# Kernel optimization log

Hardware: AMD Instinct MI355X
Metric: run time of the kernel (lower is better)

## Reference

```python
import jax, jax.numpy as jnp
import numpy as np

B, T, V, E, H, LAT, L = 2048, 120, 64, 128, 512, 256, 2


def setup_inputs() -> dict:
    key = jax.random.key(0)
    ks = jax.random.split(key, 16)
    s = 0.05  # weight init scale
    z = jax.random.normal(ks[0], (B, LAT), jnp.float32)
    target = jax.random.randint(ks[1], (B, T), 0, V)
    embed = (jax.random.normal(ks[2], (V, E), jnp.float32) * s).at[0].set(0.0)  # padding_idx=0
    fc_hidden_w = jax.random.normal(ks[3], (H * L, LAT), jnp.float32) * s
    fc_hidden_b = jax.random.normal(ks[4], (H * L,), jnp.float32) * s
    W_ih0 = jax.random.normal(ks[5], (3 * H, E + LAT), jnp.float32) * s
    W_hh0 = jax.random.normal(ks[6], (3 * H, H), jnp.float32) * s
    b_ih0 = jax.random.normal(ks[7], (3 * H,), jnp.float32) * s
    b_hh0 = jax.random.normal(ks[8], (3 * H,), jnp.float32) * s
    W_ih1 = jax.random.normal(ks[9], (3 * H, H), jnp.float32) * s
    W_hh1 = jax.random.normal(ks[10], (3 * H, H), jnp.float32) * s
    b_ih1 = jax.random.normal(ks[11], (3 * H,), jnp.float32) * s
    b_hh1 = jax.random.normal(ks[12], (3 * H,), jnp.float32) * s
    fc_out_w = jax.random.normal(ks[13], (V, H), jnp.float32) * s
    fc_out_b = jax.random.normal(ks[14], (V,), jnp.float32) * s
    return dict(z=z, target=target, embed=embed, fc_hidden_w=fc_hidden_w,
                fc_hidden_b=fc_hidden_b, W_ih0=W_ih0, W_hh0=W_hh0, b_ih0=b_ih0,
                b_hh0=b_hh0, W_ih1=W_ih1, W_hh1=W_hh1, b_ih1=b_ih1, b_hh1=b_hh1,
                fc_out_w=fc_out_w, fc_out_b=fc_out_b)


def _gru_cell(x, h, W_ih, W_hh, b_ih, b_hh):
    # torch GRU cell: r,z,n gate ordering
    gx = x @ W_ih.T + b_ih          # [B, 3H]
    gh = h @ W_hh.T + b_hh          # [B, 3H]
    xr, xz, xn = jnp.split(gx, 3, axis=-1)
    hr, hz, hn = jnp.split(gh, 3, axis=-1)
    r = jax.nn.sigmoid(xr + hr)
    u = jax.nn.sigmoid(xz + hz)
    n = jnp.tanh(xn + r * hn)
    return (1.0 - u) * n + u * h


def reference(z, target, embed, fc_hidden_w, fc_hidden_b, W_ih0, W_hh0, b_ih0,
              b_hh0, W_ih1, W_hh1, b_ih1, b_hh1, fc_out_w, fc_out_b):
    b, lat = z.shape
    t = target.shape[1]
    hd = W_hh0.shape[1]
    # initial hidden: fc_hidden(z).view(B, L, H) -> per-layer states
    hid = (z @ fc_hidden_w.T + fc_hidden_b).reshape(b, L, hd)
    h0, h1 = hid[:, 0, :], hid[:, 1, :]
    # teacher forcing with ratio 1.0: input_0 = token 1, input_t = target[:, t-1]
    tok = jnp.concatenate([jnp.ones((b, 1), target.dtype), target[:, :-1]], axis=1)
    # precompute per-step GRU inputs: [T, B, E+LAT]
    xs = jnp.concatenate(
        [embed[tok], jnp.broadcast_to(z[:, None, :], (b, t, lat))], axis=-1)
    xs = jnp.swapaxes(xs, 0, 1)

    def step(carry, x):
        h0, h1 = carry
        h0n = _gru_cell(x, h0, W_ih0, W_hh0, b_ih0, b_hh0)
        h1n = _gru_cell(h0n, h1, W_ih1, W_hh1, b_ih1, b_hh1)
        logits = h1n @ fc_out_w.T + fc_out_b
        return (h0n, h1n), logits

    _, out = jax.lax.scan(step, (h0, h1), xs)   # [T, B, V]
    return jnp.swapaxes(out, 0, 1)              # [B, T, V]
```

## Files before the change

kernel.cpp:

```cpp
#include <hip/hip_runtime.h>
#include <hip/hip_bf16.h>

#define DI __device__ __forceinline__

typedef short bf16x8 __attribute__((ext_vector_type(8)));
typedef float f32x4 __attribute__((ext_vector_type(4)));

constexpr int B_ = 2048, T_ = 120, V_ = 64, E_ = 128, H_ = 512, LAT_ = 256;
constexpr int H3 = 1536;

DI short f2b(float f) {
  union { __hip_bfloat16 h; short s; } u;
  u.h = __float2bfloat16(f);
  return u.s;
}
DI float b2f(short s) {
  union { unsigned u; float f; } x;
  x.u = (unsigned)(unsigned short)s << 16;
  return x.f;
}
DI float sigm(float x) { return 1.f / (1.f + __expf(-x)); }
DI float tanh_f(float x) {
  x = fminf(15.f, fmaxf(-15.f, x));
  float e = __expf(2.f * x);
  return (e - 1.f) / (e + 1.f);
}
DI float gru_one(float xr, float xz, float xn, float hr, float hz, float hn, float hp) {
  float r = sigm(xr + hr);
  float u = sigm(xz + hz);
  float nn = tanh_f(xn + r * hn);
  return (1.f - u) * nn + u * hp;
}
DI float gru_pre(float sr, float sz, float xn, float hn, float hp) {
  float r = sigm(sr);
  float u = sigm(sz);
  float nn = tanh_f(xn + r * hn);
  return (1.f - u) * nn + u * hp;
}

template <int ROWS, int BK, int NV>
DI void rs_load(const short* __restrict__ G, int row0, int K, int kk, bf16x8 (&v)[NV]) {
  constexpr int SLOTS = BK / 8;
  constexpr int RPP = 2048 / BK;
  static_assert(NV == ROWS / RPP, "NV mismatch");
  const int tid = threadIdx.x;
  const int rl = tid / SLOTS, sl = tid % SLOTS;
#pragma unroll
  for (int p = 0; p < NV; ++p)
    v[p] = *(const bf16x8*)(G + (size_t)(row0 + p * RPP + rl) * K + kk + sl * 8);
}
template <int ROWS, int BK, int NV>
DI void rs_write(char* __restrict__ lds, bf16x8 (&v)[NV]) {
  constexpr int SLOTS = BK / 8;
  constexpr int RPP = 2048 / BK;
  const int tid = threadIdx.x;
  const int rl = tid / SLOTS, sl = tid % SLOTS;
#pragma unroll
  for (int p = 0; p < NV; ++p) {
    int row = p * RPP + rl;
    *(bf16x8*)(lds + row * (SLOTS * 16) + ((sl ^ (row & (SLOTS - 1))) * 16)) = v[p];
  }
}
template <int BK>
DI bf16x8 fragL(const char* __restrict__ lds, int row, int kk) {
  return *(const bf16x8*)(lds + row * (BK * 2) + ((kk << 1) ^ ((row & (BK / 8 - 1)) << 4)));
}

DI void gemm_core(const short* __restrict__ A, const short* __restrict__ Bw,
                  int arow, int bcol, char* lds, f32x4 (&acc)[2][4]) {
  char* As[2] = {lds, lds + 8192};
  char* Bs[2] = {lds + 16384, lds + 32768};
  const int tid = threadIdx.x, lane = tid & 63, wid = tid >> 6;
  const int wm = wid >> 1, wn = wid & 1;
  const int r = lane & 15, ko = (lane >> 4) * 8;
  bf16x8 va[2], vb[4];
  rs_load<64, 64, 2>(A, arow, H_, 0, va);
  rs_load<128, 64, 4>(Bw, bcol, H_, 0, vb);
  rs_write<64, 64, 2>(As[0], va);
  rs_write<128, 64, 4>(Bs[0], vb);
  __syncthreads();
  int cur = 0;
  for (int c = 0; c < 8; ++c) {
    if (c < 7) {
      rs_load<64, 64, 2>(A, arow, H_, (c + 1) * 64, va);
      rs_load<128, 64, 4>(Bw, bcol, H_, (c + 1) * 64, vb);
    }
#pragma unroll
    for (int kh = 0; kh < 2; ++kh) {
      const int kkk = kh * 32 + ko;
      bf16x8 a[2], b[4];
#pragma unroll
      for (int i = 0; i < 2; ++i) a[i] = fragL<64>(As[cur], wm * 32 + i * 16 + r, kkk);
#pragma unroll
      for (int j = 0; j < 4; ++j) b[j] = fragL<64>(Bs[cur], wn * 64 + j * 16 + r, kkk);
#pragma unroll
      for (int i = 0; i < 2; ++i)
#pragma unroll
        for (int j = 0; j < 4; ++j)
          acc[i][j] = __builtin_amdgcn_mfma_f32_16x16x32_bf16(a[i], b[j], acc[i][j], 0, 0, 0);
    }
    if (c < 7) {
      rs_write<64, 64, 2>(As[cur ^ 1], va);
      rs_write<128, 64, 4>(Bs[cur ^ 1], vb);
    }
    __syncthreads();
    cur ^= 1;
  }
}

struct GArgs {
  const short* zgx; const short* egx; const int* target;
  float* h0f; float* h1f; short* h0b; short* h1b;
  short* p0;
  short* gx1a; short* gx1b;
  short* gh1;
  const short* Wb_hh0; const float* b_hh0;
  const short* Wb_ih1; const float* b_ih1;
  const short* Wb_hh1; const float* b_hh1;
  const short* Wb_out; const float* fc_out_b;
  float* out;
};

__global__ __launch_bounds__(256) void k_A(GArgs a, int t) {
  extern __shared__ char smem[];
  const int u = blockIdx.x;
  const int tid = threadIdx.x, lane = tid & 63, wid = tid >> 6;
  if (u < 384) {
    if (t >= T_) return;
    const int mt = u / 12, nt = u % 12;
    const int arow = mt * 64, bcol = nt * 128;
    f32x4 acc[2][4] = {};
    gemm_core(a.h0b, a.Wb_hh0, arow, bcol, smem, acc);
    const int wm = wid >> 1, wn = wid & 1;
    const int r0 = (lane >> 4) * 4, c0 = lane & 15;
    const int g = nt >> 2;
#pragma unroll
    for (int i = 0; i < 2; ++i)
#pragma unroll
      for (int j = 0; j < 4; ++j) {
        const int col = bcol + wn * 64 + j * 16 + c0;
        const int jj = col & 511;
        const float bv = a.b_hh0[col];
#pragma unroll
        for (int rr = 0; rr < 4; ++rr) {
          const int row = arow + wm * 32 + i * 16 + r0 + rr;
          const float val = acc[i][j][rr] + bv;
          const int tok = (t == 0) ? 1 : a.target[(size_t)row * T_ + (t - 1)];
          const float xv = b2f(a.zgx[(size_t)row * H3 + g * 512 + jj]) +
                           b2f(a.egx[(size_t)tok * H3 + g * 512 + jj]);
          short* pr = a.p0 + ((size_t)row * 4) * 512 + jj;
          if (g < 2) {
            pr[g * 512] = f2b(val + xv);
          } else {
            pr[2 * 512] = f2b(xv);
            pr[3 * 512] = f2b(val);
          }
        }
      }
    return;
  }
  if (u < 768) {
    if (t < 1 || t > T_) return;
    short* gxw = ((t - 1) & 1) ? a.gx1b : a.gx1a;
    const int uu = u - 384;
    const int mt = uu / 12, nt = uu % 12;
    const int arow = mt * 64, bcol = nt * 128;
    f32x4 acc[2][4] = {};
    gemm_core(a.h0b, a.Wb_ih1, arow, bcol, smem, acc);
    const int wm = wid >> 1, wn = wid & 1;
    const int r0 = (lane >> 4) * 4, c0 = lane & 15;
#pragma unroll
    for (int i = 0; i < 2; ++i)
#pragma unroll
      for (int j = 0; j < 4; ++j) {
        const int col = bcol + wn * 64 + j * 16 + c0;
        const float bv = a.b_ih1[col];
#pragma unroll
        for (int rr = 0; rr < 4; ++rr)
          gxw[(size_t)(arow + wm * 32 + i * 16 + r0 + rr) * H3 + col] = f2b(acc[i][j][rr] + bv);
      }
    return;
  }
  if (t < 2) return;
  const short* gxr = (t & 1) ? a.gx1b : a.gx1a;
  short* sh = (short*)smem;
  const int row0 = (u - 768) * 16;
  const int tlog = t - 2;
#pragma unroll 1
  for (int c = 0; c < 4; ++c) {
    int f = c * 2048 + tid * 8;
    int rl = f >> 9, j = f & 511;
    int row = row0 + rl;
    const short* gx = gxr + (size_t)row * H3 + j;
    const short* gh = a.gh1 + (size_t)row * H3 + j;
    float* hf = a.h1f + (size_t)row * H_ + j;
    bf16x8 xr = *(const bf16x8*)(gx);
    bf16x8 xz = *(const bf16x8*)(gx + H_);
    bf16x8 xn = *(const bf16x8*)(gx + 2 * H_);
    bf16x8 hr = *(const bf16x8*)(gh);
    bf16x8 hz = *(const bf16x8*)(gh + H_);
    bf16x8 hn = *(const bf16x8*)(gh + 2 * H_);
    float4 hp0 = *(const float4*)(hf);
    float4 hp1 = *(const float4*)(hf + 4);
    float hp[8] = {hp0.x, hp0.y, hp0.z, hp0.w, hp1.x, hp1.y, hp1.z, hp1.w};
    float hv[8];
    bf16x8 ov;
#pragma unroll
    for (int e = 0; e < 8; ++e) {
      hv[e] = gru_one(b2f(xr[e]), b2f(xz[e]), b2f(xn[e]),
                      b2f(hr[e]), b2f(hz[e]), b2f(hn[e]), hp[e]);
      ov[e] = f2b(hv[e]);
    }
    *(float4*)(hf) = make_float4(hv[0], hv[1], hv[2], hv[3]);
    *(float4*)(hf + 4) = make_float4(hv[4], hv[5], hv[6], hv[7]);
    *(bf16x8*)(a.h1b + (size_t)row * H_ + j) = ov;
    *(bf16x8*)(&sh[rl * 520 + j]) = ov;
  }
  __syncthreads();
  const int w = tid >> 6;
  const int c0 = lane & 15, ko = (lane >> 4) * 8;
  f32x4 acc = {};
  const short* wb = a.Wb_out + (size_t)(w * 16 + c0) * H_ + ko;
  const short* ap = &sh[c0 * 520 + ko];
#pragma unroll
  for (int m = 0; m < 16; ++m) {
    bf16x8 av = *(const bf16x8*)(ap + m * 32);
    bf16x8 bw = *(const bf16x8*)(wb + m * 32);
    acc = __builtin_amdgcn_mfma_f32_16x16x32_bf16(av, bw, acc, 0, 0, 0);
  }
  const int r0 = (lane >> 4) * 4;
  const int col = w * 16 + c0;
  const float bv = a.fc_out_b[col];
#pragma unroll
  for (int rr = 0; rr < 4; ++rr) {
    int brow = row0 + r0 + rr;
    a.out[((size_t)brow * T_ + tlog) * V_ + col] = acc[rr] + bv;
  }
}

__global__ __launch_bounds__(256) void k_C(GArgs a, int t) {
  extern __shared__ char smem[];
  const int u = blockIdx.x;
  const int tid = threadIdx.x;
  if (u < 128) {
    if (t >= T_) return;
    const int row0 = u * 16;
#pragma unroll 1
    for (int it = 0; it < 4; ++it) {
      int v = it * 256 + tid;
      int rl = v >> 6, jb = v & 63;
      int row = row0 + rl, j = jb * 8;
      const short* pr = a.p0 + ((size_t)row * 4) * 512 + j;
      bf16x8 sr = *(const bf16x8*)(pr);
      bf16x8 sz = *(const bf16x8*)(pr + 512);
      bf16x8 xn = *(const bf16x8*)(pr + 1024);
      bf16x8 hn = *(const bf16x8*)(pr + 1536);
      float* hf = a.h0f + (size_t)row * H_ + j;
      float4 hp0 = *(const float4*)(hf);
      float4 hp1 = *(const float4*)(hf + 4);
      float hp[8] = {hp0.x, hp0.y, hp0.z, hp0.w, hp1.x, hp1.y, hp1.z, hp1.w};
      float hv[8];
      bf16x8 ov;
#pragma unroll
      for (int e = 0; e < 8; ++e) {
        hv[e] = gru_pre(b2f(sr[e]), b2f(sz[e]), b2f(xn[e]), b2f(hn[e]), hp[e]);
        ov[e] = f2b(hv[e]);
      }
      *(float4*)(hf) = make_float4(hv[0], hv[1], hv[2], hv[3]);
      *(float4*)(hf + 4) = make_float4(hv[4], hv[5], hv[6], hv[7]);
      *(bf16x8*)(a.h0b + (size_t)row * H_ + j) = ov;
    }
    return;
  }
  if (t < 1 || t > T_) return;
  const int uu = u - 128;
  const int mt = uu / 12, nt = uu % 12;
  const int arow = mt * 64, bcol = nt * 128;
  f32x4 acc[2][4] = {};
  gemm_core(a.h1b, a.Wb_hh1, arow, bcol, smem, acc);
  const int lane = tid & 63, wid = tid >> 6;
  const int wm = wid >> 1, wn = wid & 1;
  const int r0 = (lane >> 4) * 4, c0 = lane & 15;
#pragma unroll
  for (int i = 0; i < 2; ++i)
#pragma unroll
    for (int j = 0; j < 4; ++j) {
      const int col = bcol + wn * 64 + j * 16 + c0;
      const float bv = a.b_hh1[col];
#pragma unroll
      for (int rr = 0; rr < 4; ++rr)
        a.gh1[(size_t)(arow + wm * 32 + i * 16 + r0 + rr) * H3 + col] = f2b(acc[i][j][rr] + bv);
    }
}

template <int MI, int NJ>
DI void gemm_wave_global(const short* __restrict__ A, const short* __restrict__ B,
                         const int K, const int arow, const int bcol,
                         f32x4 (&acc)[MI][NJ]) {
  const int lane = threadIdx.x & 63;
  const int r = lane & 15, ko = (lane >> 4) * 8;
  const short* Ap = A + (size_t)(arow + r) * K + ko;
  const short* Bp = B + (size_t)(bcol + r) * K + ko;
  for (int kk = 0; kk < K; kk += 32) {
    bf16x8 a[MI], b[NJ];
#pragma unroll
    for (int i = 0; i < MI; ++i) a[i] = *(const bf16x8*)(Ap + (size_t)i * 16 * K + kk);
#pragma unroll
    for (int j = 0; j < NJ; ++j) b[j] = *(const bf16x8*)(Bp + (size_t)j * 16 * K + kk);
#pragma unroll
    for (int i = 0; i < MI; ++i)
#pragma unroll
      for (int j = 0; j < NJ; ++j)
        acc[i][j] = __builtin_amdgcn_mfma_f32_16x16x32_bf16(a[i], b[j], acc[i][j], 0, 0, 0);
  }
}
template <int MI, int NJ>
DI void epi_store_bf16(short* __restrict__ C, const float* __restrict__ bias,
                       const int N, const int arow, const int bcol, f32x4 (&acc)[MI][NJ]) {
  const int lane = threadIdx.x & 63;
  const int r0 = (lane >> 4) * 4, c0 = lane & 15;
#pragma unroll
  for (int i = 0; i < MI; ++i)
#pragma unroll
    for (int j = 0; j < NJ; ++j) {
      int col = bcol + j * 16 + c0;
      float bv = bias[col];
#pragma unroll
      for (int rr = 0; rr < 4; ++rr)
        C[(size_t)(arow + i * 16 + r0 + rr) * N + col] = f2b(acc[i][j][rr] + bv);
    }
}

__global__ __launch_bounds__(256) void k_prep0(
    const float* __restrict__ W_hh0, const float* __restrict__ W_ih1,
    const float* __restrict__ W_hh1, const float* __restrict__ fc_out_w,
    const float* __restrict__ W_ih0, const float* __restrict__ fc_hidden_w,
    const float* __restrict__ z,
    short* Wb_hh0, short* Wb_ih1, short* Wb_hh1, short* Wb_out,
    short* Wb_ih0z, short* Wb_fch, short* z_b) {
  const int n1 = H3 * H_;
  const int n2 = V_ * H_;
  const int n3 = H3 * LAT_;
  const int n4 = (2 * H_) * LAT_;
  const int n5 = B_ * LAT_;
  const int total = n1 * 3 + n2 + n3 + n4 + n5;
  for (int i = blockIdx.x * blockDim.x + threadIdx.x; i < total;
       i += gridDim.x * blockDim.x) {
    int idx = i;
    if (idx < n1) { Wb_hh0[idx] = f2b(W_hh0[idx]); continue; }
    idx -= n1;
    if (idx < n1) { Wb_ih1[idx] = f2b(W_ih1[idx]); continue; }
    idx -= n1;
    if (idx < n1) { Wb_hh1[idx] = f2b(W_hh1[idx]); continue; }
    idx -= n1;
    if (idx < n2) { Wb_out[idx] = f2b(fc_out_w[idx]); continue; }
    idx -= n2;
    if (idx < n3) {
      int n = idx >> 8, k = idx & 255;
      Wb_ih0z[idx] = f2b(W_ih0[(size_t)n * (E_ + LAT_) + E_ + k]);
      continue;
    }
    idx -= n3;
    if (idx < n4) { Wb_fch[idx] = f2b(fc_hidden_w[idx]); continue; }
    idx -= n4;
    z_b[idx] = f2b(z[idx]);
  }
}

__global__ __launch_bounds__(256) void k_prep_emb(const float* __restrict__ embed,
                                                  const float* __restrict__ W_ih0,
                                                  short* __restrict__ egx) {
  __shared__ float er[E_];
  int v = blockIdx.x;
  for (int e = threadIdx.x; e < E_; e += blockDim.x) er[e] = embed[(size_t)v * E_ + e];
  __syncthreads();
  for (int n = threadIdx.x; n < H3; n += blockDim.x) {
    const float* w = W_ih0 + (size_t)n * (E_ + LAT_);
    float acc = 0.f;
#pragma unroll 8
    for (int e = 0; e < E_; ++e) acc += er[e] * w[e];
    egx[(size_t)v * H3 + n] = f2b(acc);
  }
}

__global__ __launch_bounds__(256) void k_prep1(
    const short* __restrict__ z_b, const short* __restrict__ Wb_ih0z,
    const short* __restrict__ Wb_fch, const float* __restrict__ b_ih0,
    const float* __restrict__ fc_hidden_b,
    short* zgx, float* h0f, float* h1f, short* h0b, short* h1b) {
  const int bid = blockIdx.x;
  const int mtile = bid / 20, ntile = bid % 20;
  const int tid = threadIdx.x, lane = tid & 63, wid = tid >> 6;
  const int wm = wid >> 1, wn = wid & 1;
  const int arow = mtile * 128 + wm * 64;
  f32x4 acc[4][4] = {};
  if (ntile < 12) {
    int bcol = ntile * 128 + wn * 64;
    gemm_wave_global<4, 4>(z_b, Wb_ih0z, LAT_, arow, bcol, acc);
    epi_store_bf16<4, 4>(zgx, b_ih0, H3, arow, bcol, acc);
  } else {
    int bcol = (ntile - 12) * 128 + wn * 64;
    gemm_wave_global<4, 4>(z_b, Wb_fch, LAT_, arow, bcol, acc);
    const int r0 = (lane >> 4) * 4, c0 = lane & 15;
#pragma unroll
    for (int i = 0; i < 4; ++i)
#pragma unroll
      for (int j = 0; j < 4; ++j) {
        int col = bcol + j * 16 + c0;
        float bv = fc_hidden_b[col];
#pragma unroll
        for (int rr = 0; rr < 4; ++rr) {
          int row = arow + i * 16 + r0 + rr;
          float v = acc[i][j][rr] + bv;
          if (col < H_) {
            h0f[(size_t)row * H_ + col] = v;
            h0b[(size_t)row * H_ + col] = f2b(v);
          } else {
            h1f[(size_t)row * H_ + (col - H_)] = v;
            h1b[(size_t)row * H_ + (col - H_)] = f2b(v);
          }
        }
      }
  }
}

extern "C" void kernel_launch(void* const* d_in, const int* in_sizes, int n_in,
                              void* d_out, int out_size, void* d_ws, size_t ws_size,
                              hipStream_t stream) {
  const float* z           = (const float*)d_in[0];
  const int*   target      = (const int*)d_in[1];
  const float* embed       = (const float*)d_in[2];
  const float* fc_hidden_w = (const float*)d_in[3];
  const float* fc_hidden_b = (const float*)d_in[4];
  const float* W_ih0       = (const float*)d_in[5];
  const float* W_hh0       = (const float*)d_in[6];
  const float* b_ih0       = (const float*)d_in[7];
  const float* b_hh0       = (const float*)d_in[8];
  const float* W_ih1       = (const float*)d_in[9];
  const float* W_hh1       = (const float*)d_in[10];
  const float* b_ih1       = (const float*)d_in[11];
  const float* b_hh1       = (const float*)d_in[12];
  const float* fc_out_w    = (const float*)d_in[13];
  const float* fc_out_b    = (const float*)d_in[14];
  float* out = (float*)d_out;

  char* ws = (char*)d_ws;
  size_t off = 0;
  auto alloc = [&](size_t bytes) -> void* {
    off = (off + 255) & ~(size_t)255;
    void* p = ws + off;
    off += bytes;
    return p;
  };
  float* h0f    = (float*)alloc((size_t)B_ * H_ * 4);
  float* h1f    = (float*)alloc((size_t)B_ * H_ * 4);
  short* h0b    = (short*)alloc((size_t)B_ * H_ * 2);
  short* h1b    = (short*)alloc((size_t)B_ * H_ * 2);
  short* p0     = (short*)alloc((size_t)B_ * 4 * H_ * 2);
  short* gx1a   = (short*)alloc((size_t)B_ * H3 * 2);
  short* gx1b   = (short*)alloc((size_t)B_ * H3 * 2);
  short* gh1    = (short*)alloc((size_t)B_ * H3 * 2);
  short* zgx    = (short*)alloc((size_t)B_ * H3 * 2);
  short* egx    = (short*)alloc((size_t)V_ * H3 * 2);
  short* Wb_hh0 = (short*)alloc((size_t)H3 * H_ * 2);
  short* Wb_ih1 = (short*)alloc((size_t)H3 * H_ * 2);
  short* Wb_hh1 = (short*)alloc((size_t)H3 * H_ * 2);
  short* Wb_out = (short*)alloc((size_t)V_ * H_ * 2);
  short* Wb_ih0z= (short*)alloc((size_t)H3 * LAT_ * 2);
  short* Wb_fch = (short*)alloc((size_t)2 * H_ * LAT_ * 2);
  short* z_b    = (short*)alloc((size_t)B_ * LAT_ * 2);
  if (off > ws_size) return;

  k_prep0<<<2048, 256, 0, stream>>>(W_hh0, W_ih1, W_hh1, fc_out_w, W_ih0, fc_hidden_w,
                                    z, Wb_hh0, Wb_ih1, Wb_hh1, Wb_out, Wb_ih0z, Wb_fch, z_b);
  k_prep_emb<<<64, 256, 0, stream>>>(embed, W_ih0, egx);
  k_prep1<<<320, 256, 0, stream>>>(z_b, Wb_ih0z, Wb_fch, b_ih0, fc_hidden_b,
                                   zgx, h0f, h1f, h0b, h1b);

  GArgs a;
  a.zgx = zgx; a.egx = egx; a.target = target;
  a.h0f = h0f; a.h1f = h1f; a.h0b = h0b; a.h1b = h1b;
  a.p0 = p0; a.gx1a = gx1a; a.gx1b = gx1b; a.gh1 = gh1;
  a.Wb_hh0 = Wb_hh0; a.b_hh0 = b_hh0;
  a.Wb_ih1 = Wb_ih1; a.b_ih1 = b_ih1;
  a.Wb_hh1 = Wb_hh1; a.b_hh1 = b_hh1;
  a.Wb_out = Wb_out; a.fc_out_b = fc_out_b;
  a.out = out;

  for (int t = 0; t <= T_ + 1; ++t) {
    k_A<<<896, 256, 49152, stream>>>(a, t);
    if (t <= T_) k_C<<<512, 256, 49152, stream>>>(a, t);
  }
}
```

Measured before the change: 4.389 ms.

## Restructure recurrent schedule into two per-step kernels, dropping gx1 double buffer

The per-timestep work is regrouped so one kernel runs all three GEMMs (hh0, ih1, hh1), with the layer-0 GEMM pairs interleaved per row group. The second kernel does the layer-0 and layer-1 pointwise GRU updates plus the output projection. The pipeline lag shrinks from two steps to one, so the loop runs one fewer iteration and the double-buffered gx1 becomes a single buffer. The second kernel uses only 256 blocks and a smaller shared allocation. Merging the three GEMMs into a 1152-block launch raises per-launch parallelism, at the cost of a different dependency staging between layers.

```diff
diff --git a/kernel.cpp b/kernel.cpp
--- a/kernel.cpp
+++ b/kernel.cpp
@@ -112,8 +112,7 @@
   const short* zgx; const short* egx; const int* target;
   float* h0f; float* h1f; short* h0b; short* h1b;
   short* p0;
-  short* gx1a; short* gx1b;
-  short* gh1;
+  short* gx1; short* gh1;
   const short* Wb_hh0; const float* b_hh0;
   const short* Wb_ih1; const float* b_ih1;
   const short* Wb_hh1; const float* b_hh1;
@@ -121,124 +120,83 @@
   float* out;
 };
 
-__global__ __launch_bounds__(256) void k_A(GArgs a, int t) {
+__global__ __launch_bounds__(256) void k_L1(GArgs a, int t) {
   extern __shared__ char smem[];
   const int u = blockIdx.x;
   const int tid = threadIdx.x, lane = tid & 63, wid = tid >> 6;
-  if (u < 384) {
-    if (t >= T_) return;
-    const int mt = u / 12, nt = u % 12;
-    const int arow = mt * 64, bcol = nt * 128;
-    f32x4 acc[2][4] = {};
-    gemm_core(a.h0b, a.Wb_hh0, arow, bcol, smem, acc);
-    const int wm = wid >> 1, wn = wid & 1;
-    const int r0 = (lane >> 4) * 4, c0 = lane & 15;
-    const int g = nt >> 2;
-#pragma unroll
-    for (int i = 0; i < 2; ++i)
-#pragma unroll
-      for (int j = 0; j < 4; ++j) {
-        const int col = bcol + wn * 64 + j * 16 + c0;
-        const int jj = col & 511;
-        const float bv = a.b_hh0[col];
-#pragma unroll
-        for (int rr = 0; rr < 4; ++rr) {
-          const int row = arow + wm * 32 + i * 16 + r0 + rr;
-          const float val = acc[i][j][rr] + bv;
-          const int tok = (t == 0) ? 1 : a.target[(size_t)row * T_ + (t - 1)];
-          const float xv = b2f(a.zgx[(size_t)row * H3 + g * 512 + jj]) +
-                           b2f(a.egx[(size_t)tok * H3 + g * 512 + jj]);
-          short* pr = a.p0 + ((size_t)row * 4) * 512 + jj;
-          if (g < 2) {
-            pr[g * 512] = f2b(val + xv);
-          } else {
-            pr[2 * 512] = f2b(xv);
-            pr[3 * 512] = f2b(val);
+  const int wm = wid >> 1, wn = wid & 1;
+  const int r0 = (lane >> 4) * 4, c0 = lane & 15;
+  if (u < 768) {
+    const int grp = u / 24;
+    const int rem = u % 24;
+    const int nt = rem % 12;
+    const int arow = grp * 64, bcol = nt * 128;
+    if (rem < 12) {
+      if (t >= T_) return;
+      f32x4 acc[2][4] = {};
+      gemm_core(a.h0b, a.Wb_hh0, arow, bcol, smem, acc);
+      const int g = nt >> 2;
+#pragma unroll
+      for (int i = 0; i < 2; ++i)
+#pragma unroll
+        for (int j = 0; j < 4; ++j) {
+          const int col = bcol + wn * 64 + j * 16 + c0;
+          const int jj = col & 511;
+          const float bv = a.b_hh0[col];
+#pragma unroll
+          for (int rr = 0; rr < 4; ++rr) {
+            const int row = arow + wm * 32 + i * 16 + r0 + rr;
+            const float val = acc[i][j][rr] + bv;
+            const int tok = (t == 0) ? 1 : a.target[(size_t)row * T_ + (t - 1)];
+            const float xv = b2f(a.zgx[(size_t)row * H3 + g * 512 + jj]) +
+                             b2f(a.egx[(size_t)tok * H3 + g * 512 + jj]);
+            short* pr = a.p0 + ((size_t)row * 4) * 512 + jj;
+            if (g < 2) {
+              pr[g * 512] = f2b(val + xv);
+            } else {
+              pr[2 * 512] = f2b(xv);
+              pr[3 * 512] = f2b(val);
+            }
           }
         }
-      }
+    } else {
+      if (t < 1) return;
+      f32x4 acc[2][4] = {};
+      gemm_core(a.h0b, a.Wb_ih1, arow, bcol, smem, acc);
+#pragma unroll
+      for (int i = 0; i < 2; ++i)
+#pragma unroll
+        for (int j = 0; j < 4; ++j) {
+          const int col = bcol + wn * 64 + j * 16 + c0;
+          const float bv = a.b_ih1[col];
+#pragma unroll
+          for (int rr = 0; rr < 4; ++rr)
+            a.gx1[(size_t)(arow + wm * 32 + i * 16 + r0 + rr) * H3 + col] =
+                f2b(acc[i][j][rr] + bv);
+        }
+    }
     return;
   }
-  if (u < 768) {
-    if (t < 1 || t > T_) return;
-    short* gxw = ((t - 1) & 1) ? a.gx1b : a.gx1a;
-    const int uu = u - 384;
-    const int mt = uu / 12, nt = uu % 12;
-    const int arow = mt * 64, bcol = nt * 128;
-    f32x4 acc[2][4] = {};
-    gemm_core(a.h0b, a.Wb_ih1, arow, bcol, smem, acc);
-    const int wm = wid >> 1, wn = wid & 1;
-    const int r0 = (lane >> 4) * 4, c0 = lane & 15;
-#pragma unroll
-    for (int i = 0; i < 2; ++i)
-#pragma unroll
-      for (int j = 0; j < 4; ++j) {
-        const int col = bcol + wn * 64 + j * 16 + c0;
-        const float bv = a.b_ih1[col];
-#pragma unroll
-        for (int rr = 0; rr < 4; ++rr)
-          gxw[(size_t)(arow + wm * 32 + i * 16 + r0 + rr) * H3 + col] = f2b(acc[i][j][rr] + bv);
-      }
-    return;
-  }
-  if (t < 2) return;
-  const short* gxr = (t & 1) ? a.gx1b : a.gx1a;
-  short* sh = (short*)smem;
-  const int row0 = (u - 768) * 16;
-  const int tlog = t - 2;
-#pragma unroll 1
-  for (int c = 0; c < 4; ++c) {
-    int f = c * 2048 + tid * 8;
-    int rl = f >> 9, j = f & 511;
-    int row = row0 + rl;
-    const short* gx = gxr + (size_t)row * H3 + j;
-    const short* gh = a.gh1 + (size_t)row * H3 + j;
-    float* hf = a.h1f + (size_t)row * H_ + j;
-    bf16x8 xr = *(const bf16x8*)(gx);
-    bf16x8 xz = *(const bf16x8*)(gx + H_);
-    bf16x8 xn = *(const bf16x8*)(gx + 2 * H_);
-    bf16x8 hr = *(const bf16x8*)(gh);
-    bf16x8 hz = *(const bf16x8*)(gh + H_);
-    bf16x8 hn = *(const bf16x8*)(gh + 2 * H_);
-    float4 hp0 = *(const float4*)(hf);
-    float4 hp1 = *(const float4*)(hf + 4);
-    float hp[8] = {hp0.x, hp0.y, hp0.z, hp0.w, hp1.x, hp1.y, hp1.z, hp1.w};
-    float hv[8];
-    bf16x8 ov;
-#pragma unroll
-    for (int e = 0; e < 8; ++e) {
-      hv[e] = gru_one(b2f(xr[e]), b2f(xz[e]), b2f(xn[e]),
-                      b2f(hr[e]), b2f(hz[e]), b2f(hn[e]), hp[e]);
-      ov[e] = f2b(hv[e]);
-    }
-    *(float4*)(hf) = make_float4(hv[0], hv[1], hv[2], hv[3]);
-    *(float4*)(hf + 4) = make_float4(hv[4], hv[5], hv[6], hv[7]);
-    *(bf16x8*)(a.h1b + (size_t)row * H_ + j) = ov;
-    *(bf16x8*)(&sh[rl * 520 + j]) = ov;
-  }
-  __syncthreads();
-  const int w = tid >> 6;
-  const int c0 = lane & 15, ko = (lane >> 4) * 8;
-  f32x4 acc = {};
-  const short* wb = a.Wb_out + (size_t)(w * 16 + c0) * H_ + ko;
-  const short* ap = &sh[c0 * 520 + ko];
-#pragma unroll
-  for (int m = 0; m < 16; ++m) {
-    bf16x8 av = *(const bf16x8*)(ap + m * 32);
-    bf16x8 bw = *(const bf16x8*)(wb + m * 32);
-    acc = __builtin_amdgcn_mfma_f32_16x16x32_bf16(av, bw, acc, 0, 0, 0);
-  }
-  const int r0 = (lane >> 4) * 4;
-  const int col = w * 16 + c0;
-  const float bv = a.fc_out_b[col];
-#pragma unroll
-  for (int rr = 0; rr < 4; ++rr) {
-    int brow = row0 + r0 + rr;
-    a.out[((size_t)brow * T_ + tlog) * V_ + col] = acc[rr] + bv;
-  }
-}
-
-__global__ __launch_bounds__(256) void k_C(GArgs a, int t) {
+  if (t < 1) return;
+  const int uu = u - 768;
+  const int mt = uu / 12, nt = uu % 12;
+  const int arow = mt * 64, bcol = nt * 128;
+  f32x4 acc[2][4] = {};
+  gemm_core(a.h1b, a.Wb_hh1, arow, bcol, smem, acc);
+#pragma unroll
+  for (int i = 0; i < 2; ++i)
+#pragma unroll
+    for (int j = 0; j < 4; ++j) {
+      const int col = bcol + wn * 64 + j * 16 + c0;
+      const float bv = a.b_hh1[col];
+#pragma unroll
+      for (int rr = 0; rr < 4; ++rr)
+        a.gh1[(size_t)(arow + wm * 32 + i * 16 + r0 + rr) * H3 + col] =
+            f2b(acc[i][j][rr] + bv);
+    }
+}
+
+__global__ __launch_bounds__(256) void k_L2(GArgs a, int t) {
   extern __shared__ char smem[];
   const int u = blockIdx.x;
   const int tid = threadIdx.x;
@@ -272,25 +230,60 @@
     }
     return;
   }
-  if (t < 1 || t > T_) return;
-  const int uu = u - 128;
-  const int mt = uu / 12, nt = uu % 12;
-  const int arow = mt * 64, bcol = nt * 128;
-  f32x4 acc[2][4] = {};
-  gemm_core(a.h1b, a.Wb_hh1, arow, bcol, smem, acc);
-  const int lane = tid & 63, wid = tid >> 6;
-  const int wm = wid >> 1, wn = wid & 1;
-  const int r0 = (lane >> 4) * 4, c0 = lane & 15;
-#pragma unroll
-  for (int i = 0; i < 2; ++i)
-#pragma unroll
-    for (int j = 0; j < 4; ++j) {
-      const int col = bcol + wn * 64 + j * 16 + c0;
-      const float bv = a.b_hh1[col];
-#pragma unroll
-      for (int rr = 0; rr < 4; ++rr)
-        a.gh1[(size_t)(arow + wm * 32 + i * 16 + r0 + rr) * H3 + col] = f2b(acc[i][j][rr] + bv);
-    }
+  if (t < 1) return;
+  short* sh = (short*)smem;
+  const int row0 = (u - 128) * 16;
+  const int tlog = t - 1;
+#pragma unroll 1
+  for (int c = 0; c < 4; ++c) {
+    int f = c * 2048 + tid * 8;
+    int rl = f >> 9, j = f & 511;
+    int row = row0 + rl;
+    const short* gx = a.gx1 + (size_t)row * H3 + j;
+    const short* gh = a.gh1 + (size_t)row * H3 + j;
+    float* hf = a.h1f + (size_t)row * H_ + j;
+    bf16x8 xr = *(const bf16x8*)(gx);
+    bf16x8 xz = *(const bf16x8*)(gx + H_);
+    bf16x8 xn = *(const bf16x8*)(gx + 2 * H_);
+    bf16x8 hr = *(const bf16x8*)(gh);
+    bf16x8 hz = *(const bf16x8*)(gh + H_);
+    bf16x8 hn = *(const bf16x8*)(gh + 2 * H_);
+    float4 hp0 = *(const float4*)(hf);
+    float4 hp1 = *(const float4*)(hf + 4);
+    float hp[8] = {hp0.x, hp0.y, hp0.z, hp0.w, hp1.x, hp1.y, hp1.z, hp1.w};
+    float hv[8];
+    bf16x8 ov;
+#pragma unroll
+    for (int e = 0; e < 8; ++e) {
+      hv[e] = gru_one(b2f(xr[e]), b2f(xz[e]), b2f(xn[e]),
+                      b2f(hr[e]), b2f(hz[e]), b2f(hn[e]), hp[e]);
+      ov[e] = f2b(hv[e]);
+    }
+    *(float4*)(hf) = make_float4(hv[0], hv[1], hv[2], hv[3]);
+    *(float4*)(hf + 4) = make_float4(hv[4], hv[5], hv[6], hv[7]);
+    *(bf16x8*)(a.h1b + (size_t)row * H_ + j) = ov;
+    *(bf16x8*)(&sh[rl * 520 + j]) = ov;
+  }
+  __syncthreads();
+  const int lane = tid & 63, w = tid >> 6;
+  const int c0 = lane & 15, ko = (lane >> 4) * 8;
+  f32x4 acc = {};
+  const short* wb = a.Wb_out + (size_t)(w * 16 + c0) * H_ + ko;
+  const short* ap = &sh[c0 * 520 + ko];
+#pragma unroll
+  for (int m = 0; m < 16; ++m) {
+    bf16x8 av = *(const bf16x8*)(ap + m * 32);
+    bf16x8 bw = *(const bf16x8*)(wb + m * 32);
+    acc = __builtin_amdgcn_mfma_f32_16x16x32_bf16(av, bw, acc, 0, 0, 0);
+  }
+  const int r0 = (lane >> 4) * 4;
+  const int col = w * 16 + c0;
+  const float bv = a.fc_out_b[col];
+#pragma unroll
+  for (int rr = 0; rr < 4; ++rr) {
+    int brow = row0 + r0 + rr;
+    a.out[((size_t)brow * T_ + tlog) * V_ + col] = acc[rr] + bv;
+  }
 }
 
 template <int MI, int NJ>
@@ -457,8 +450,7 @@
   short* h0b    = (short*)alloc((size_t)B_ * H_ * 2);
   short* h1b    = (short*)alloc((size_t)B_ * H_ * 2);
   short* p0     = (short*)alloc((size_t)B_ * 4 * H_ * 2);
-  short* gx1a   = (short*)alloc((size_t)B_ * H3 * 2);
-  short* gx1b   = (short*)alloc((size_t)B_ * H3 * 2);
+  short* gx1    = (short*)alloc((size_t)B_ * H3 * 2);
   short* gh1    = (short*)alloc((size_t)B_ * H3 * 2);
   short* zgx    = (short*)alloc((size_t)B_ * H3 * 2);
   short* egx    = (short*)alloc((size_t)V_ * H3 * 2);
@@ -480,15 +472,15 @@
   GArgs a;
   a.zgx = zgx; a.egx = egx; a.target = target;
   a.h0f = h0f; a.h1f = h1f; a.h0b = h0b; a.h1b = h1b;
-  a.p0 = p0; a.gx1a = gx1a; a.gx1b = gx1b; a.gh1 = gh1;
+  a.p0 = p0; a.gx1 = gx1; a.gh1 = gh1;
   a.Wb_hh0 = Wb_hh0; a.b_hh0 = b_hh0;
   a.Wb_ih1 = Wb_ih1; a.b_ih1 = b_ih1;
   a.Wb_hh1 = Wb_hh1; a.b_hh1 = b_hh1;
   a.Wb_out = Wb_out; a.fc_out_b = fc_out_b;
   a.out = out;
 
-  for (int t = 0; t <= T_ + 1; ++t) {
-    k_A<<<896, 256, 49152, stream>>>(a, t);
-    if (t <= T_) k_C<<<512, 256, 49152, stream>>>(a, t);
-  }
-}
+  for (int t = 0; t <= T_; ++t) {
+    k_L1<<<1152, 256, 49152, stream>>>(a, t);
+    k_L2<<<256, 256, 16640, stream>>>(a, t);
+  }
+}
```

Result: slower. 4.647 ms (+5.9%).
